# Kernel optimization log

Hardware: AMD Instinct MI355X
Metric: run time of the kernel (lower is better)

## Reference

```python
import jax, jax.numpy as jnp
import numpy as np
import math

V = 50257   # target_vocab_size
E = 512     # opt.out_embeddings_size
B = 8
L = 2048
NR = 100    # noise_ratio
NORM_TERM = math.log(V)   # norm_term='auto'
LOG_NR = math.log(NR)


def setup_inputs() -> dict:
    key = jax.random.key(0)
    k1, k2, k3, k4, k5 = jax.random.split(key, 5)
    # build_unigram_noise: counts -> probs; clamp(1e-10); renorm; log  (Zipf-like counts)
    counts = 1.0 / np.arange(1, V + 1, dtype=np.float64)
    probs = counts / counts.sum()
    probs = np.clip(probs, 1e-10, None)
    probs = probs / probs.sum()
    logprob_noise = jnp.asarray(np.log(probs), dtype=jnp.float32)
    target = jax.random.randint(k1, (B, L), 0, V)
    noise_idx = jax.random.randint(k2, (NR,), 0, V)  # shared noise (per_word=False)
    inp = jax.random.normal(k3, (B, L, E), jnp.float32) * 0.05
    emb_weight = jax.random.normal(k4, (V, E), jnp.float32) * 0.02
    bias_weight = jax.random.normal(k5, (V,), jnp.float32) * 0.01
    return {"input": inp, "emb_weight": emb_weight, "bias_weight": bias_weight,
            "logprob_noise": logprob_noise, "target": target, "noise_idx": noise_idx}


def reference(input, emb_weight, bias_weight, logprob_noise, target, noise_idx):
    # _compute_sampled_logit_batched
    flat_in = input.reshape(-1, E)                    # (B*L, E)
    tflat = target.reshape(-1)                        # (B*L,)
    t_emb = emb_weight[tflat]                         # gather (B*L, E)
    target_score = jnp.sum(flat_in * t_emb, axis=1) + bias_weight[tflat]
    n_emb = emb_weight[noise_idx]                     # (NR, E)
    noise_score = flat_in @ n_emb.T + bias_weight[noise_idx]  # (B*L, NR)
    # _get_logit: subtract norm term
    logit_t_model = target_score.reshape(B, L) - NORM_TERM
    logit_n_model = noise_score.reshape(B, L, NR) - NORM_TERM
    # noise-distribution log-probs
    logit_t_noise = logprob_noise[target]                                   # (B, L)
    logit_n_noise = jnp.broadcast_to(logprob_noise[noise_idx], (B, L, NR))  # shared
    # nce_loss
    logit_model = jnp.concatenate([logit_t_model[..., None], logit_n_model], axis=2)
    logit_noise = jnp.concatenate([logit_t_noise[..., None], logit_n_noise], axis=2)
    x = logit_model - logit_noise - LOG_NR            # (B, L, NR+1)
    # BCEWithLogits, label=1 at slot 0 else 0: loss = softplus(x) - x*y
    bce = jnp.logaddexp(0.0, x)
    bce = bce.at[:, :, 0].add(-x[:, :, 0])
    loss = bce.sum(axis=2)                            # (B, L)
    return loss.mean()                                # reduction='elementwise_mean'
```

## Files before the change

### kernel.cpp

```cpp
#include <hip/hip_runtime.h>


#define E_SZ   512
#define NROWS  16384
#define NRn    100
#define NWp    112
#define MT     16
#define NBLK   (NROWS / MT)

typedef __attribute__((ext_vector_type(8))) short short8;
typedef __attribute__((ext_vector_type(4))) float f32x4;

#define NTL 15.430077572997398f

__device__ __forceinline__ unsigned int pack2(float a, float b) {
    unsigned int ua = __float_as_uint(a) + 0x8000u;
    unsigned int ub = __float_as_uint(b) + 0x8000u;
    return __builtin_amdgcn_perm(ub, ua, 0x07060302u);
}
__device__ __forceinline__ float softplus(float x) {
    return fmaxf(x, 0.f) + log1pf(__expf(-fabsf(x)));
}
__device__ __forceinline__ short8 cvt8(float4 x0, float4 x1) {
    union { unsigned int u[4]; short8 s; } r;
    r.u[0] = pack2(x0.x, x0.y);
    r.u[1] = pack2(x0.z, x0.w);
    r.u[2] = pack2(x1.x, x1.y);
    r.u[3] = pack2(x1.z, x1.w);
    return r.s;
}

__global__ __launch_bounds__(128)
void prep_noise(const float* __restrict__ emb, const float* __restrict__ bias,
                const float* __restrict__ lpn, const int* __restrict__ nidx,
                unsigned short* __restrict__ nB,
                float* __restrict__ nBn,
                float* __restrict__ out)
{
    const int j = blockIdx.x;
    const int t = threadIdx.x;
    const int idx = (j < NRn) ? nidx[j] : 0;
    float4 v = {0.f, 0.f, 0.f, 0.f};
    if (j < NRn) v = *(const float4*)(emb + (size_t)idx * E_SZ + t * 4);
    unsigned int u0 = pack2(v.x, v.y);
    unsigned int u1 = pack2(v.z, v.w);
    const int kg  = t >> 1;
    const int off = (t & 1) * 4;
    *(uint2*)(nB + ((size_t)kg * NWp + j) * 8 + off) = make_uint2(u0, u1);
    if (t == 0)
        nBn[j] = (j < NRn) ? (bias[idx] - NTL - lpn[idx]) : 0.f;
    if (j == 0 && t == 0)
        out[0] = 0.f;
}

__global__ __launch_bounds__(256, 4)
void nce_loss_kernel(const float* __restrict__ inp,
                     const float* __restrict__ emb,
                     const float* __restrict__ bias,
                     const float* __restrict__ lpn,
                     const int*   __restrict__ target,
                     const unsigned short* __restrict__ nB,
                     const float* __restrict__ nBn,
                     float* __restrict__ out)
{
    const int t    = threadIdx.x;
    const int w    = t >> 6;
    const int lane = t & 63;
    const int c    = lane & 15;
    const int q    = lane >> 4;
    const int r0   = blockIdx.x * MT;

    __shared__ float sAcc[4 * 2048];
    __shared__ float sBn[NWp];
    __shared__ float sTb[MT];
    __shared__ float sWs[4];

    if (t < NWp) sBn[t] = nBn[t];
    if (t < MT) {
        int tg = target[r0 + t];
        sTb[t] = bias[tg] - NTL - lpn[tg];
    }

    const int kb = w * 128 + q * 8;
    const float* pA = inp + (size_t)(r0 + c) * E_SZ + kb;
    const float* pT = emb + (size_t)target[r0 + c] * E_SZ + kb;
    const unsigned short* pB = nB + ((size_t)(w * 16 + q) * NWp + c) * 8;

    f32x4 accN[7];
    f32x4 accT = {0.f, 0.f, 0.f, 0.f};
#pragma unroll
    for (int ti = 0; ti < 7; ++ti) accN[ti] = {0.f, 0.f, 0.f, 0.f};

    short8 curB[7];
#pragma unroll
    for (int ti = 0; ti < 7; ++ti) curB[ti] = *(const short8*)(pB + ti * 128);

    float4 a[2][2], tt[2][2];
#pragma unroll
    for (int p = 0; p < 2; ++p) {
        a[p][0]  = *(const float4*)(pA + p * 32);
        a[p][1]  = *(const float4*)(pA + p * 32 + 4);
        tt[p][0] = *(const float4*)(pT + p * 32);
        tt[p][1] = *(const float4*)(pT + p * 32 + 4);
    }

#pragma unroll
    for (int ks = 0; ks < 4; ++ks) {
        const int pb = ks & 1;
        short8 A = cvt8(a[pb][0], a[pb][1]);
        short8 T = cvt8(tt[pb][0], tt[pb][1]);
        short8 Bv[7];
#pragma unroll
        for (int ti = 0; ti < 7; ++ti) Bv[ti] = curB[ti];

        if (ks < 2) {
            a[pb][0]  = *(const float4*)(pA + (ks + 2) * 32);
            a[pb][1]  = *(const float4*)(pA + (ks + 2) * 32 + 4);
            tt[pb][0] = *(const float4*)(pT + (ks + 2) * 32);
            tt[pb][1] = *(const float4*)(pT + (ks + 2) * 32 + 4);
        }
        if (ks < 3) {
            const unsigned short* pBn = pB + (size_t)(ks + 1) * 4 * NWp * 8;
#pragma unroll
            for (int ti = 0; ti < 7; ++ti)
                curB[ti] = *(const short8*)(pBn + ti * 128);
        }

        accT = __builtin_amdgcn_mfma_f32_16x16x32_bf16(A, T, accT, 0, 0, 0);
#pragma unroll
        for (int ti = 0; ti < 7; ++ti)
            accN[ti] = __builtin_amdgcn_mfma_f32_16x16x32_bf16(A, Bv[ti], accN[ti], 0, 0, 0);
    }

    float* slab = sAcc + w * 2048;
#pragma unroll
    for (int ti = 0; ti < 7; ++ti)
#pragma unroll
        for (int r = 0; r < 4; ++r)
            slab[ti * 256 + r * 64 + lane] = accN[ti][r];
#pragma unroll
    for (int r = 0; r < 4; ++r)
        slab[7 * 256 + r * 64 + lane] = accT[r];
    __syncthreads();

    const int ereg = w;
    const int col  = lane & 15;
    const int erow = (lane >> 4) * 4 + ereg;
    float ll = 0.f;
#pragma unroll
    for (int i = 0; i < 7; ++i) {
        int word = i * 16 + col;
        float v = sAcc[i * 256 + t] + sAcc[2048 + i * 256 + t]
                + sAcc[4096 + i * 256 + t] + sAcc[6144 + i * 256 + t];
        if (word < NRn)
            ll += softplus(v + sBn[word]);
    }
    {
        float v = sAcc[7 * 256 + t] + sAcc[2048 + 7 * 256 + t]
                + sAcc[4096 + 7 * 256 + t] + sAcc[6144 + 7 * 256 + t];
        if (col == erow)
            ll += softplus(-(v + sTb[erow]));
    }

#pragma unroll
    for (int off = 32; off > 0; off >>= 1) ll += __shfl_down(ll, off);
    if (lane == 0) sWs[w] = ll;
    __syncthreads();
    if (t == 0) {
        float s = (sWs[0] + sWs[1]) + (sWs[2] + sWs[3]);
        atomicAdd(out, s * (1.f / (float)NROWS));
    }
}

extern "C" void kernel_launch(void* const* d_in, const int* in_sizes, int n_in,
                              void* d_out, int out_size, void* d_ws, size_t ws_size,
                              hipStream_t stream) {
    const float* inp    = (const float*)d_in[0];
    const float* emb    = (const float*)d_in[1];
    const float* bias   = (const float*)d_in[2];
    const float* lpn    = (const float*)d_in[3];
    const int*   target = (const int*)d_in[4];
    const int*   nidx   = (const int*)d_in[5];
    float* out = (float*)d_out;

    unsigned short* nB  = (unsigned short*)d_ws;
    float*          nBn = (float*)((char*)d_ws + (size_t)64 * NWp * 8 * 2);

    prep_noise<<<NWp, 128, 0, stream>>>(emb, bias, lpn, nidx, nB, nBn, out);
    nce_loss_kernel<<<NBLK, 256, 0, stream>>>(inp, emb, bias, lpn, target, nB, nBn, out);
}
```

Before: 177.8 us.

## Stage bf16 A/target tiles in LDS with coalesced loads and atomic split-K reduce

Instead of each lane loading scattered 8-float slices of input and target embeddings, threads now load contiguous 16-float row segments, convert them to bf16 and store them to padded LDS tiles in two K chunks. The MFMA operands are then read from LDS. The four per-wave accumulator slabs are replaced by one shared buffer reduced with LDS atomicAdd, which cuts shared memory and allows the occupancy hint to rise from 4 to 5 blocks. The cost is extra __syncthreads, the loss of register prefetch overlap, and serialized LDS atomics.

```diff
diff --git a/kernel.cpp b/kernel.cpp
--- a/kernel.cpp
+++ b/kernel.cpp
@@ -7,6 +7,7 @@
 #define NWp    112
 #define MT     16
 #define NBLK   (NROWS / MT)
+#define SASTR  264
 
 typedef __attribute__((ext_vector_type(8))) short short8;
 typedef __attribute__((ext_vector_type(4))) float f32x4;
@@ -53,7 +54,7 @@
         out[0] = 0.f;
 }
 
-__global__ __launch_bounds__(256, 4)
+__global__ __launch_bounds__(256, 5)
 void nce_loss_kernel(const float* __restrict__ inp,
                      const float* __restrict__ emb,
                      const float* __restrict__ bias,
@@ -70,94 +71,93 @@
     const int q    = lane >> 4;
     const int r0   = blockIdx.x * MT;
 
-    __shared__ float sAcc[4 * 2048];
+    __shared__ __align__(16) unsigned short sA[MT * SASTR];
+    __shared__ __align__(16) unsigned short sT[MT * SASTR];
+    __shared__ float sAccS[2048];
     __shared__ float sBn[NWp];
     __shared__ float sTb[MT];
+    __shared__ int   sTg[MT];
     __shared__ float sWs[4];
 
+    for (int i = t; i < 2048; i += 256) sAccS[i] = 0.f;
     if (t < NWp) sBn[t] = nBn[t];
     if (t < MT) {
         int tg = target[r0 + t];
+        sTg[t] = tg;
         sTb[t] = bias[tg] - NTL - lpn[tg];
     }
+    __syncthreads();
 
-    const int kb = w * 128 + q * 8;
-    const float* pA = inp + (size_t)(r0 + c) * E_SZ + kb;
-    const float* pT = emb + (size_t)target[r0 + c] * E_SZ + kb;
-    const unsigned short* pB = nB + ((size_t)(w * 16 + q) * NWp + c) * 8;
+    const int srow = t >> 4;
+    const int sseg = t & 15;
+    const float* gA = inp + (size_t)(r0 + srow) * E_SZ + sseg * 16;
+    const float* gT = emb + (size_t)sTg[srow] * E_SZ + sseg * 16;
+    unsigned short* wA = sA + srow * SASTR + sseg * 16;
+    unsigned short* wT = sT + srow * SASTR + sseg * 16;
 
     f32x4 accN[7];
     f32x4 accT = {0.f, 0.f, 0.f, 0.f};
 #pragma unroll
     for (int ti = 0; ti < 7; ++ti) accN[ti] = {0.f, 0.f, 0.f, 0.f};
 
-    short8 curB[7];
+#pragma unroll 1
+    for (int ck = 0; ck < 2; ++ck) {
+        {
+            float4 a0 = *(const float4*)(gA + ck * 256);
+            float4 a1 = *(const float4*)(gA + ck * 256 + 4);
+            float4 a2 = *(const float4*)(gA + ck * 256 + 8);
+            float4 a3 = *(const float4*)(gA + ck * 256 + 12);
+            float4 t0 = *(const float4*)(gT + ck * 256);
+            float4 t1 = *(const float4*)(gT + ck * 256 + 4);
+            float4 t2 = *(const float4*)(gT + ck * 256 + 8);
+            float4 t3 = *(const float4*)(gT + ck * 256 + 12);
+            *(short8*)(wA)     = cvt8(a0, a1);
+            *(short8*)(wA + 8) = cvt8(a2, a3);
+            *(short8*)(wT)     = cvt8(t0, t1);
+            *(short8*)(wT + 8) = cvt8(t2, t3);
+        }
+        __syncthreads();
+
 #pragma unroll
-    for (int ti = 0; ti < 7; ++ti) curB[ti] = *(const short8*)(pB + ti * 128);
-
-    float4 a[2][2], tt[2][2];
+        for (int ks = 0; ks < 2; ++ks) {
+            const int ko = w * 64 + ks * 32 + q * 8;
+            const unsigned short* pBk =
+                nB + ((size_t)(ck * 32 + w * 8 + ks * 4 + q) * NWp + c) * 8;
+            short8 Bv[7];
 #pragma unroll
-    for (int p = 0; p < 2; ++p) {
-        a[p][0]  = *(const float4*)(pA + p * 32);
-        a[p][1]  = *(const float4*)(pA + p * 32 + 4);
-        tt[p][0] = *(const float4*)(pT + p * 32);
-        tt[p][1] = *(const float4*)(pT + p * 32 + 4);
+            for (int ti = 0; ti < 7; ++ti) Bv[ti] = *(const short8*)(pBk + ti * 128);
+            short8 A = *(const short8*)&sA[c * SASTR + ko];
+            short8 T = *(const short8*)&sT[c * SASTR + ko];
+            accT = __builtin_amdgcn_mfma_f32_16x16x32_bf16(A, T, accT, 0, 0, 0);
+#pragma unroll
+            for (int ti = 0; ti < 7; ++ti)
+                accN[ti] = __builtin_amdgcn_mfma_f32_16x16x32_bf16(A, Bv[ti], accN[ti], 0, 0, 0);
+        }
+        __syncthreads();
     }
 
-#pragma unroll
-    for (int ks = 0; ks < 4; ++ks) {
-        const int pb = ks & 1;
-        short8 A = cvt8(a[pb][0], a[pb][1]);
-        short8 T = cvt8(tt[pb][0], tt[pb][1]);
-        short8 Bv[7];
-#pragma unroll
-        for (int ti = 0; ti < 7; ++ti) Bv[ti] = curB[ti];
-
-        if (ks < 2) {
-            a[pb][0]  = *(const float4*)(pA + (ks + 2) * 32);
-            a[pb][1]  = *(const float4*)(pA + (ks + 2) * 32 + 4);
-            tt[pb][0] = *(const float4*)(pT + (ks + 2) * 32);
-            tt[pb][1] = *(const float4*)(pT + (ks + 2) * 32 + 4);
-        }
-        if (ks < 3) {
-            const unsigned short* pBn = pB + (size_t)(ks + 1) * 4 * NWp * 8;
-#pragma unroll
-            for (int ti = 0; ti < 7; ++ti)
-                curB[ti] = *(const short8*)(pBn + ti * 128);
-        }
-
-        accT = __builtin_amdgcn_mfma_f32_16x16x32_bf16(A, T, accT, 0, 0, 0);
-#pragma unroll
-        for (int ti = 0; ti < 7; ++ti)
-            accN[ti] = __builtin_amdgcn_mfma_f32_16x16x32_bf16(A, Bv[ti], accN[ti], 0, 0, 0);
-    }
-
-    float* slab = sAcc + w * 2048;
 #pragma unroll
     for (int ti = 0; ti < 7; ++ti)
 #pragma unroll
         for (int r = 0; r < 4; ++r)
-            slab[ti * 256 + r * 64 + lane] = accN[ti][r];
+            atomicAdd(&sAccS[ti * 256 + r * 64 + lane], accN[ti][r]);
 #pragma unroll
     for (int r = 0; r < 4; ++r)
-        slab[7 * 256 + r * 64 + lane] = accT[r];
+        atomicAdd(&sAccS[7 * 256 + r * 64 + lane], accT[r]);
     __syncthreads();
 
-    const int ereg = w;
     const int col  = lane & 15;
-    const int erow = (lane >> 4) * 4 + ereg;
+    const int erow = (lane >> 4) * 4 + w;
     float ll = 0.f;
 #pragma unroll
     for (int i = 0; i < 7; ++i) {
+        float v = sAccS[i * 256 + t];
         int word = i * 16 + col;
-        float v = sAcc[i * 256 + t] + sAcc[2048 + i * 256 + t]
-                + sAcc[4096 + i * 256 + t] + sAcc[6144 + i * 256 + t];
         if (word < NRn)
             ll += softplus(v + sBn[word]);
     }
     {
-        float v = sAcc[7 * 256 + t] + sAcc[2048 + 7 * 256 + t]
-                + sAcc[4096 + 7 * 256 + t] + sAcc[6144 + 7 * 256 + t];
+        float v = sAccS[7 * 256 + t];
         if (col == erow)
             ll += softplus(-(v + sTb[erow]));
     }
```

Measured after the change: 218.2 us. +22.8%, slower.

## Split noise columns across two block groups and reduce K-partials with LDS atomics

Applied to the files above, without the earlier changes.

The grid is doubled. One group of blocks computes the target dot product plus the first four noise-word tiles, and the other group computes the remaining three noise tiles. The 32KB per-wave accumulation slab is replaced by an 8KB shared buffer that waves add into with LDS atomics. Launch bounds are raised to allow more resident blocks. This aims at more parallelism and occupancy, at the cost of reading the input rows twice and doing serialized shared-memory atomic adds.

```diff
diff --git a/kernel.cpp b/kernel.cpp
--- a/kernel.cpp
+++ b/kernel.cpp
@@ -53,7 +53,7 @@
         out[0] = 0.f;
 }
 
-__global__ __launch_bounds__(256, 4)
+__global__ __launch_bounds__(256, 6)
 void nce_loss_kernel(const float* __restrict__ inp,
                      const float* __restrict__ emb,
                      const float* __restrict__ bias,
@@ -68,98 +68,154 @@
     const int lane = t & 63;
     const int c    = lane & 15;
     const int q    = lane >> 4;
-    const int r0   = blockIdx.x * MT;
-
-    __shared__ float sAcc[4 * 2048];
+    const bool g0  = (blockIdx.x < NBLK);
+    const int r0   = (g0 ? blockIdx.x : blockIdx.x - NBLK) * MT;
+
+    __shared__ float sAccS[2048];
     __shared__ float sBn[NWp];
     __shared__ float sTb[MT];
     __shared__ float sWs[4];
 
+    for (int i = t; i < 2048; i += 256) sAccS[i] = 0.f;
     if (t < NWp) sBn[t] = nBn[t];
-    if (t < MT) {
+    if (g0 && t < MT) {
         int tg = target[r0 + t];
         sTb[t] = bias[tg] - NTL - lpn[tg];
     }
 
     const int kb = w * 128 + q * 8;
     const float* pA = inp + (size_t)(r0 + c) * E_SZ + kb;
-    const float* pT = emb + (size_t)target[r0 + c] * E_SZ + kb;
     const unsigned short* pB = nB + ((size_t)(w * 16 + q) * NWp + c) * 8;
 
-    f32x4 accN[7];
-    f32x4 accT = {0.f, 0.f, 0.f, 0.f};
-#pragma unroll
-    for (int ti = 0; ti < 7; ++ti) accN[ti] = {0.f, 0.f, 0.f, 0.f};
-
-    short8 curB[7];
-#pragma unroll
-    for (int ti = 0; ti < 7; ++ti) curB[ti] = *(const short8*)(pB + ti * 128);
-
-    float4 a[2][2], tt[2][2];
-#pragma unroll
-    for (int p = 0; p < 2; ++p) {
-        a[p][0]  = *(const float4*)(pA + p * 32);
-        a[p][1]  = *(const float4*)(pA + p * 32 + 4);
-        tt[p][0] = *(const float4*)(pT + p * 32);
-        tt[p][1] = *(const float4*)(pT + p * 32 + 4);
-    }
-
-#pragma unroll
-    for (int ks = 0; ks < 4; ++ks) {
-        const int pb = ks & 1;
-        short8 A = cvt8(a[pb][0], a[pb][1]);
-        short8 T = cvt8(tt[pb][0], tt[pb][1]);
-        short8 Bv[7];
-#pragma unroll
-        for (int ti = 0; ti < 7; ++ti) Bv[ti] = curB[ti];
-
-        if (ks < 2) {
-            a[pb][0]  = *(const float4*)(pA + (ks + 2) * 32);
-            a[pb][1]  = *(const float4*)(pA + (ks + 2) * 32 + 4);
-            tt[pb][0] = *(const float4*)(pT + (ks + 2) * 32);
-            tt[pb][1] = *(const float4*)(pT + (ks + 2) * 32 + 4);
-        }
-        if (ks < 3) {
-            const unsigned short* pBn = pB + (size_t)(ks + 1) * 4 * NWp * 8;
-#pragma unroll
-            for (int ti = 0; ti < 7; ++ti)
-                curB[ti] = *(const short8*)(pBn + ti * 128);
-        }
-
-        accT = __builtin_amdgcn_mfma_f32_16x16x32_bf16(A, T, accT, 0, 0, 0);
-#pragma unroll
-        for (int ti = 0; ti < 7; ++ti)
-            accN[ti] = __builtin_amdgcn_mfma_f32_16x16x32_bf16(A, Bv[ti], accN[ti], 0, 0, 0);
-    }
-
-    float* slab = sAcc + w * 2048;
-#pragma unroll
-    for (int ti = 0; ti < 7; ++ti)
+    float ll = 0.f;
+
+    if (g0) {
+        const float* pT = emb + (size_t)target[r0 + c] * E_SZ + kb;
+
+        f32x4 accN[4];
+        f32x4 accT = {0.f, 0.f, 0.f, 0.f};
+#pragma unroll
+        for (int ti = 0; ti < 4; ++ti) accN[ti] = {0.f, 0.f, 0.f, 0.f};
+
+        short8 curB[4];
+#pragma unroll
+        for (int ti = 0; ti < 4; ++ti) curB[ti] = *(const short8*)(pB + ti * 128);
+
+        float4 a[2][2], tt[2][2];
+#pragma unroll
+        for (int p = 0; p < 2; ++p) {
+            a[p][0]  = *(const float4*)(pA + p * 32);
+            a[p][1]  = *(const float4*)(pA + p * 32 + 4);
+            tt[p][0] = *(const float4*)(pT + p * 32);
+            tt[p][1] = *(const float4*)(pT + p * 32 + 4);
+        }
+
+#pragma unroll
+        for (int ks = 0; ks < 4; ++ks) {
+            const int pb = ks & 1;
+            short8 A = cvt8(a[pb][0], a[pb][1]);
+            short8 T = cvt8(tt[pb][0], tt[pb][1]);
+            short8 Bv[4];
+#pragma unroll
+            for (int ti = 0; ti < 4; ++ti) Bv[ti] = curB[ti];
+
+            if (ks < 2) {
+                a[pb][0]  = *(const float4*)(pA + (ks + 2) * 32);
+                a[pb][1]  = *(const float4*)(pA + (ks + 2) * 32 + 4);
+                tt[pb][0] = *(const float4*)(pT + (ks + 2) * 32);
+                tt[pb][1] = *(const float4*)(pT + (ks + 2) * 32 + 4);
+            }
+            if (ks < 3) {
+                const unsigned short* pBn = pB + (size_t)(ks + 1) * 4 * NWp * 8;
+#pragma unroll
+                for (int ti = 0; ti < 4; ++ti)
+                    curB[ti] = *(const short8*)(pBn + ti * 128);
+            }
+
+            accT = __builtin_amdgcn_mfma_f32_16x16x32_bf16(A, T, accT, 0, 0, 0);
+#pragma unroll
+            for (int ti = 0; ti < 4; ++ti)
+                accN[ti] = __builtin_amdgcn_mfma_f32_16x16x32_bf16(A, Bv[ti], accN[ti], 0, 0, 0);
+        }
+
+        __syncthreads();
+#pragma unroll
+        for (int ti = 0; ti < 4; ++ti)
+#pragma unroll
+            for (int r = 0; r < 4; ++r)
+                atomicAdd(&sAccS[ti * 256 + r * 64 + lane], accN[ti][r]);
 #pragma unroll
         for (int r = 0; r < 4; ++r)
-            slab[ti * 256 + r * 64 + lane] = accN[ti][r];
-#pragma unroll
-    for (int r = 0; r < 4; ++r)
-        slab[7 * 256 + r * 64 + lane] = accT[r];
-    __syncthreads();
-
-    const int ereg = w;
-    const int col  = lane & 15;
-    const int erow = (lane >> 4) * 4 + ereg;
-    float ll = 0.f;
-#pragma unroll
-    for (int i = 0; i < 7; ++i) {
-        int word = i * 16 + col;
-        float v = sAcc[i * 256 + t] + sAcc[2048 + i * 256 + t]
-                + sAcc[4096 + i * 256 + t] + sAcc[6144 + i * 256 + t];
-        if (word < NRn)
-            ll += softplus(v + sBn[word]);
-    }
-    {
-        float v = sAcc[7 * 256 + t] + sAcc[2048 + 7 * 256 + t]
-                + sAcc[4096 + 7 * 256 + t] + sAcc[6144 + 7 * 256 + t];
-        if (col == erow)
-            ll += softplus(-(v + sTb[erow]));
+            atomicAdd(&sAccS[7 * 256 + r * 64 + lane], accT[r]);
+        __syncthreads();
+
+        const int col  = lane & 15;
+        const int erow = (lane >> 4) * 4 + w;
+#pragma unroll
+        for (int i = 0; i < 4; ++i) {
+            int word = i * 16 + col;
+            ll += softplus(sAccS[i * 256 + t] + sBn[word]);
+        }
+        {
+            float v = sAccS[7 * 256 + t];
+            if (col == erow)
+                ll += softplus(-(v + sTb[erow]));
+        }
+    } else {
+        f32x4 accN[3];
+#pragma unroll
+        for (int ti = 0; ti < 3; ++ti) accN[ti] = {0.f, 0.f, 0.f, 0.f};
+
+        short8 curB[3];
+#pragma unroll
+        for (int ti = 0; ti < 3; ++ti) curB[ti] = *(const short8*)(pB + (4 + ti) * 128);
+
+        float4 a[2][2];
+#pragma unroll
+        for (int p = 0; p < 2; ++p) {
+            a[p][0] = *(const float4*)(pA + p * 32);
+            a[p][1] = *(const float4*)(pA + p * 32 + 4);
+        }
+
+#pragma unroll
+        for (int ks = 0; ks < 4; ++ks) {
+            const int pb = ks & 1;
+            short8 A = cvt8(a[pb][0], a[pb][1]);
+            short8 Bv[3];
+#pragma unroll
+            for (int ti = 0; ti < 3; ++ti) Bv[ti] = curB[ti];
+
+            if (ks < 2) {
+                a[pb][0] = *(const float4*)(pA + (ks + 2) * 32);
+                a[pb][1] = *(const float4*)(pA + (ks + 2) * 32 + 4);
+            }
+            if (ks < 3) {
+                const unsigned short* pBn = pB + (size_t)(ks + 1) * 4 * NWp * 8;
+#pragma unroll
+                for (int ti = 0; ti < 3; ++ti)
+                    curB[ti] = *(const short8*)(pBn + (4 + ti) * 128);
+            }
+
+#pragma unroll
+            for (int ti = 0; ti < 3; ++ti)
+                accN[ti] = __builtin_amdgcn_mfma_f32_16x16x32_bf16(A, Bv[ti], accN[ti], 0, 0, 0);
+        }
+
+        __syncthreads();
+#pragma unroll
+        for (int ti = 0; ti < 3; ++ti)
+#pragma unroll
+            for (int r = 0; r < 4; ++r)
+                atomicAdd(&sAccS[(4 + ti) * 256 + r * 64 + lane], accN[ti][r]);
+        __syncthreads();
+
+        const int col = lane & 15;
+#pragma unroll
+        for (int i = 4; i < 7; ++i) {
+            int word = i * 16 + col;
+            if (word < NRn)
+                ll += softplus(sAccS[i * 256 + t] + sBn[word]);
+        }
     }
 
 #pragma unroll
@@ -187,5 +243,5 @@
     float*          nBn = (float*)((char*)d_ws + (size_t)64 * NWp * 8 * 2);
 
     prep_noise<<<NWp, 128, 0, stream>>>(emb, bias, lpn, nidx, nB, nBn, out);
-    nce_loss_kernel<<<NBLK, 256, 0, stream>>>(inp, emb, bias, lpn, target, nB, nBn, out);
-}
+    nce_loss_kernel<<<2 * NBLK, 256, 0, stream>>>(inp, emb, bias, lpn, target, nB, nBn, out);
+}
```

Result: slower. 220.2 us (+23.8%).
